# Kernel optimization log

Hardware: AMD Instinct MI355X
Metric: run time of the kernel (lower is better)

Reference implementation:

```python
import jax, jax.numpy as jnp
import numpy as np

B, T, E = 4, 2048, 1024
H, HS = 16, 64

def setup_inputs() -> dict:
    key = jax.random.key(0)
    ks = jax.random.split(key, 6)
    return {
        "x": jax.random.normal(ks[0], (B, T, E), dtype=jnp.float32),
        "Wq": jax.random.normal(ks[1], (H, E, HS), dtype=jnp.float32) * 0.02,
        "Wk": jax.random.normal(ks[2], (H, E, HS), dtype=jnp.float32) * 0.02,
        "Wv": jax.random.normal(ks[3], (H, E, HS), dtype=jnp.float32) * 0.02,
        "proj_w": jax.random.normal(ks[4], (E, H * HS), dtype=jnp.float32) * 0.02,
        "proj_b": jax.random.normal(ks[5], (E,), dtype=jnp.float32) * 0.02,
    }

def reference(x, Wq, Wk, Wv, proj_w, proj_b):
    b, t, e = x.shape
    h, _, hs = Wq.shape
    # NOTE: original uses .view() (raw reshape, not transpose) from [b,t,h,hs]
    # to [h,b,t,hs]; we replicate that exactly for faithfulness.
    q = jnp.einsum('bxy,iyk->bxik', x, Wq).reshape(h, b, t, hs)
    k = jnp.einsum('bxy,iyk->bxik', x, Wk).reshape(h, b, t, hs)
    v = jnp.einsum('bxy,iyk->bxik', x, Wv).reshape(h, b, t, hs)
    # scores: [h, b, t, t], scaled by 1/sqrt(head_size)
    wei = jnp.einsum('hbqd,hbkd->hbqk', q, k) * (hs ** -0.5)
    causal = jnp.tril(jnp.ones((t, t), dtype=bool))  # [t, t]
    wei = jnp.where(causal, wei, -jnp.inf)
    wei = jax.nn.softmax(wei, axis=-1)  # dropout is identity in eval
    out = jnp.einsum('hbqk,hbkd->hbqd', wei, v)
    # raw reshape [h,b,t,hs] -> [b,t,h*hs], matching torch .view()
    out = out.reshape(b, t, h * hs)
    out = out @ proj_w.T + proj_b  # nn.Linear
    return out
```

## Files before the change

### kernel.cpp

```cpp
#include <hip/hip_runtime.h>

typedef unsigned short u16;
typedef __attribute__((ext_vector_type(8))) __bf16 bf16x8;
typedef __attribute__((ext_vector_type(4))) float f32x4;
typedef __attribute__((ext_vector_type(16))) float f32x16;
typedef __attribute__((ext_vector_type(4))) unsigned short ushort4v;
typedef __attribute__((ext_vector_type(2))) unsigned uint2v;

__device__ __forceinline__ u16 f2bf(float f) {
  unsigned u = __builtin_bit_cast(unsigned, f);
  u += 0x7fffu + ((u >> 16) & 1u);
  return (u16)(u >> 16);
}

__device__ __forceinline__ float exp2_hw(float x) {
  float r; asm("v_exp_f32 %0, %1" : "=v"(r) : "v"(x)); return r;
}
__device__ __forceinline__ unsigned cvt_pk_bf16(float a, float b) {
  unsigned r; asm("v_cvt_pk_bf16_f32 %0, %1, %2" : "=v"(r) : "v"(a), "v"(b)); return r;
}

__device__ __forceinline__ void gload_lds16(const void* g, void* l) {
  __builtin_amdgcn_global_load_lds(
      (__attribute__((address_space(1))) void*)g,
      (__attribute__((address_space(3))) void*)l, 16, 0, 0);
}

__device__ __forceinline__ void BAR() {
  asm volatile("" ::: "memory");
  __builtin_amdgcn_s_barrier();
  asm volatile("" ::: "memory");
}

#define MFMA16(a, b, c) __builtin_amdgcn_mfma_f32_16x16x32_bf16(a, b, c, 0, 0, 0)
#define MFMA32(a, b, c) __builtin_amdgcn_mfma_f32_32x32x16_bf16(a, b, c, 0, 0, 0)

#define QSCALE 0.1803368801111204f


__global__ __launch_bounds__(256)
void prep_kernel(const float* __restrict__ x, const float* __restrict__ Wq,
                 const float* __restrict__ Wk, const float* __restrict__ Wv,
                 const float* __restrict__ pw, u16* __restrict__ Xb,
                 u16* __restrict__ Wcat, u16* __restrict__ PWt) {
  const int b = blockIdx.x, tid = threadIdx.x;
  if (b < 8192) {
    int i = b * 256 + tid;
    float4 v = ((const float4*)x)[i];
    union { u16 u[4]; uint2 v2; } r;
    r.u[0] = f2bf(v.x); r.u[1] = f2bf(v.y); r.u[2] = f2bf(v.z); r.u[3] = f2bf(v.w);
    ((uint2*)Xb)[i] = r.v2;
  } else if (b < 8960) {
    __shared__ u16 lds[64 * 68];
    int bb = b - 8192;
    int sel = bb >> 8, rem = bb & 255;
    int h = rem >> 4, e0 = (rem & 15) * 64;
    const float* W = (sel == 0) ? Wq : (sel == 1) ? Wk : Wv;
    const float* src = W + ((size_t)h * 1024 + e0) * 64;
#pragma unroll
    for (int i = 0; i < 4; i++) {
      int idx = i * 1024 + tid * 4;
      int e = idx >> 6, hs = idx & 63;
      float4 v = *(const float4*)&src[idx];
      u16* d = &lds[e * 68 + hs];
      d[0] = f2bf(v.x); d[1] = f2bf(v.y); d[2] = f2bf(v.z); d[3] = f2bf(v.w);
    }
    __syncthreads();
#pragma unroll
    for (int i = 0; i < 2; i++) {
      int u = i * 256 + tid;
      int hs = u >> 3, ec = u & 7;
      union { u16 q[8]; uint4 v; } ou;
#pragma unroll
      for (int e = 0; e < 8; e++) ou.q[e] = lds[(ec * 8 + e) * 68 + hs];
      size_t n = (size_t)sel * 1024 + h * 64 + hs;
      *(uint4*)&Wcat[n * 1024 + e0 + ec * 8] = ou.v;
    }
  } else {
    int i = (b - 8960) * 256 + tid;
    float4 v = ((const float4*)pw)[i];
    union { u16 u[4]; uint2 v2; } r;
    r.u[0] = f2bf(v.x); r.u[1] = f2bf(v.y); r.u[2] = f2bf(v.z); r.u[3] = f2bf(v.w);
    ((uint2*)PWt)[i] = r.v2;
  }
}


template<int OUT_BF16>
__global__ __launch_bounds__(512, 2)
void gemm3b(const u16* __restrict__ A, const u16* __restrict__ BT,
            void* __restrict__ Cout, const float* __restrict__ bias,
            int M, int N, int K, int qcols) {
  __shared__ u16 a_lds[3][128 * 64];
  __shared__ u16 b_lds[3][256 * 64];
  const int xcd = blockIdx.x & 7;
  const int local = blockIdx.x >> 3;
  const int by = xcd * 8 + (local & 7);
  const int bx = local >> 3;
  const int tid = threadIdx.x;
  const int lane = tid & 63;
  const int w = tid >> 6;
  const int wr = w >> 2, wc = w & 3;
  const int mBase = by * 128, nBase = bx * 256;
  const int l15 = lane & 15, l4 = lane >> 4;
  const int nkt = K >> 6;

  f32x4 acc[4][4] = {};

  auto STAGE_A = [&](int s, int kt) {
#pragma unroll
    for (int j = 0; j < 2; j++) {
      int e = j * 4096 + tid * 8;
      int row = e >> 6;
      int c = ((e >> 3) & 7) ^ (row & 7);
      gload_lds16(A + (size_t)(mBase + row) * K + kt * 64 + c * 8, &a_lds[s][e]);
    }
  };
  auto STAGE_B = [&](int s, int kt) {
#pragma unroll
    for (int j = 0; j < 4; j++) {
      int e = j * 4096 + tid * 8;
      int row = e >> 6;
      int c = ((e >> 3) & 7) ^ (row & 7);
      gload_lds16(BT + (size_t)(nBase + row) * K + kt * 64 + c * 8, &b_lds[s][e]);
    }
  };

  STAGE_A(0, 0); STAGE_B(0, 0);
  STAGE_A(1, 1); STAGE_B(1, 1);
  asm volatile("s_waitcnt vmcnt(6)" ::: "memory");
  BAR();

  int s0 = 0, s1 = 1, s2 = 2;
  for (int t = 0; t < nkt; t++) {
    const int t2 = (t + 2 < nkt) ? t + 2 : t + 2 - nkt;
    bf16x8 AF[4][2], BF[2][2];

#pragma unroll
    for (int m = 0; m < 4; m++) {
      int row = wr * 64 + m * 16 + l15;
#pragma unroll
      for (int ks = 0; ks < 2; ks++) {
        int ch = (ks * 4 + l4) ^ (row & 7);
        AF[m][ks] = *(const bf16x8*)&a_lds[s0][row * 64 + ch * 8];
      }
    }
#pragma unroll
    for (int n = 0; n < 2; n++) {
      int row = wc * 64 + n * 16 + l15;
#pragma unroll
      for (int ks = 0; ks < 2; ks++) {
        int ch = (ks * 4 + l4) ^ (row & 7);
        BF[n][ks] = *(const bf16x8*)&b_lds[s0][row * 64 + ch * 8];
      }
    }
    STAGE_A(s2, t2);
    BAR();
    __builtin_amdgcn_s_setprio(1);
#pragma unroll
    for (int m = 0; m < 4; m++)
#pragma unroll
      for (int n = 0; n < 2; n++) {
        acc[m][n] = MFMA16(AF[m][0], BF[n][0], acc[m][n]);
        acc[m][n] = MFMA16(AF[m][1], BF[n][1], acc[m][n]);
      }
    __builtin_amdgcn_s_setprio(0);

#pragma unroll
    for (int n = 0; n < 2; n++) {
      int row = wc * 64 + 32 + n * 16 + l15;
#pragma unroll
      for (int ks = 0; ks < 2; ks++) {
        int ch = (ks * 4 + l4) ^ (row & 7);
        BF[n][ks] = *(const bf16x8*)&b_lds[s0][row * 64 + ch * 8];
      }
    }
    STAGE_B(s2, t2);
    BAR();
    __builtin_amdgcn_s_setprio(1);
#pragma unroll
    for (int m = 0; m < 4; m++)
#pragma unroll
      for (int n = 0; n < 2; n++) {
        acc[m][2 + n] = MFMA16(AF[m][0], BF[n][0], acc[m][2 + n]);
        acc[m][2 + n] = MFMA16(AF[m][1], BF[n][1], acc[m][2 + n]);
      }
    __builtin_amdgcn_s_setprio(0);

    asm volatile("s_waitcnt vmcnt(6)" ::: "memory");
    BAR();
    int tmp = s0; s0 = s1; s1 = s2; s2 = tmp;
  }

#pragma unroll
  for (int mi = 0; mi < 4; mi++) {
    int row = mBase + wr * 64 + mi * 16 + l4 * 4;
#pragma unroll
    for (int ni = 0; ni < 4; ni++) {
      int col = nBase + wc * 64 + ni * 16 + l15;
      float scl = (col < qcols) ? QSCALE : 1.f;
#pragma unroll
      for (int j = 0; j < 4; j++) {
        float v = acc[mi][ni][j];
        if (OUT_BF16) {
          ((u16*)Cout)[(size_t)(row + j) * N + col] = f2bf(v * scl);
        } else {
          ((float*)Cout)[(size_t)(row + j) * N + col] = v + bias[col];
        }
      }
    }
  }
}


__global__ __launch_bounds__(256)
void vt_build(const u16* __restrict__ qkv, u16* __restrict__ vt) {
  __shared__ u16 lds[64 * 66];
  const int hb = blockIdx.x >> 5, tc = blockIdx.x & 31;
  const int t0 = tc * 64, tid = threadIdx.x;
#pragma unroll
  for (int i = 0; i < 2; i++) {
    int idx = i * 2048 + tid * 8;
    int tl = idx >> 6, d0 = idx & 63;
    int r = hb * 2048 + t0 + tl;
    const u16* src = &qkv[(size_t)(r >> 4) * 3072 + 2048 + (r & 15) * 64 + d0];
    uint4 v = *(const uint4*)src;
    u16* dst = &lds[tl * 66 + d0];
    *(unsigned*)(dst + 0) = v.x; *(unsigned*)(dst + 2) = v.y;
    *(unsigned*)(dst + 4) = v.z; *(unsigned*)(dst + 6) = v.w;
  }
  __syncthreads();
#pragma unroll
  for (int i = 0; i < 2; i++) {
    int idx = i * 2048 + tid * 8;
    int d = idx >> 6, tl0 = idx & 63;
    union { u16 u[8]; uint4 v; } ou;
#pragma unroll
    for (int e = 0; e < 8; e++) ou.u[e] = lds[(tl0 + e) * 66 + d];
    *(uint4*)&vt[(size_t)hb * 131072 + (size_t)d * 2048 + t0 + tl0] = ou.v;
  }
}


__global__ __launch_bounds__(256)
void attn_kernel(const u16* __restrict__ qkv, const u16* __restrict__ vtg,
                 u16* __restrict__ att) {
  __shared__ u16 k_lds[2][64 * 64];
  __shared__ u16 v_lds[2][64 * 64];

  const int xcd = blockIdx.x & 7;
  const int c = blockIdx.x >> 3;
  const int hb = xcd * 8 + (c & 7);
  const int qb = 15 - (c >> 3);
  const int tid = threadIdx.x;
  const int lane = tid & 63, w = tid >> 6;
  const int l31 = lane & 31, l5 = lane >> 5;
  const int qbase = qb * 128 + w * 32;
  const int nkt = 2 * qb + 2;

  bf16x8 qf[4];
  {
    int t = qbase + l31;
    int r = hb * 2048 + t;
    size_t base = (size_t)(r >> 4) * 3072 + (r & 15) * 64;
#pragma unroll
    for (int d = 0; d < 4; d++)
      qf[d] = *(const bf16x8*)&qkv[base + d * 16 + l5 * 8];
  }

  f32x16 o0 = {}, o1 = {};
  float lp = 0.f;

  auto STAGE = [&](int buf, int kt) {
#pragma unroll
    for (int i = 0; i < 2; i++) {
      int U = i * 2048 + tid * 8;
      int row = U >> 6;
      int chunk = ((U >> 3) & 7) ^ (row & 7);
      int rK = hb * 2048 + kt * 64 + row;
      gload_lds16(&qkv[(size_t)(rK >> 4) * 3072 + 1024 + (rK & 15) * 64 + chunk * 8],
                  &k_lds[buf][U]);
    }
#pragma unroll
    for (int i = 0; i < 2; i++) {
      int U = i * 2048 + tid * 8;
      int row = U >> 6;
      int chunk = ((U >> 3) & 7) ^ (row & 7);
      gload_lds16(&vtg[(size_t)hb * 131072 + (size_t)row * 2048 + kt * 64 + chunk * 8],
                  &v_lds[buf][U]);
    }
  };

  STAGE(0, 0);
  asm volatile("s_waitcnt vmcnt(0)" ::: "memory");
  BAR();

  for (int kt = 0; kt < nkt; kt++) {
    if (kt + 1 < nkt) STAGE((kt + 1) & 1, kt + 1);
    const int cur = kt & 1;
    const bool active = (kt * 64 <= qbase + 31);
    if (active) {
      const bool full = (kt * 64 + 63 <= qbase);
      const int q = qbase + l31;
#pragma unroll
      for (int kb = 0; kb < 2; kb++) {
        int krow = kb * 32 + l31;
        int ksw = krow & 7;
        f32x16 st = {};
        __builtin_amdgcn_s_setprio(1);
#pragma unroll
        for (int t = 0; t < 4; t++) {
          bf16x8 kf = *(const bf16x8*)&k_lds[cur][krow * 64 + ((t * 2 + l5) ^ ksw) * 8];
          st = MFMA32(kf, qf[t], st);
        }
        __builtin_amdgcn_s_setprio(0);
        float p[16];
#pragma unroll
        for (int r = 0; r < 16; r++) {
          float v = st[r];
          if (!full) {
            int k = kt * 64 + kb * 32 + (r & 3) + 8 * (r >> 2) + 4 * l5;
            v = (k > q) ? -INFINITY : v;
          }
          p[r] = exp2_hw(v);
        }
        float ps = (((p[0] + p[1]) + (p[2] + p[3])) + ((p[4] + p[5]) + (p[6] + p[7]))) +
                   (((p[8] + p[9]) + (p[10] + p[11])) + ((p[12] + p[13]) + (p[14] + p[15])));
        lp += ps;
#pragma unroll
        for (int kc = 0; kc < 2; kc++) {
          unsigned w0 = cvt_pk_bf16(p[kc * 8 + 0], p[kc * 8 + 1]);
          unsigned w1 = cvt_pk_bf16(p[kc * 8 + 2], p[kc * 8 + 3]);
          unsigned w2 = cvt_pk_bf16(p[kc * 8 + 4], p[kc * 8 + 5]);
          unsigned w3 = cvt_pk_bf16(p[kc * 8 + 6], p[kc * 8 + 7]);
          uint2v sw0 = __builtin_amdgcn_permlane32_swap(w0, w2, false, false);
          uint2v sw1 = __builtin_amdgcn_permlane32_swap(w1, w3, false, false);
          union { unsigned u[4]; bf16x8 v; } pf;
          pf.u[0] = sw0.x; pf.u[1] = sw1.x; pf.u[2] = sw0.y; pf.u[3] = sw1.y;
          __builtin_amdgcn_s_setprio(1);
          {
            int row0 = l31;
            int ch0 = (kb * 4 + kc * 2 + l5) ^ (row0 & 7);
            bf16x8 vf0 = *(const bf16x8*)&v_lds[cur][row0 * 64 + ch0 * 8];
            o0 = MFMA32(vf0, pf.v, o0);
            int row1 = 32 + l31;
            int ch1 = (kb * 4 + kc * 2 + l5) ^ (row1 & 7);
            bf16x8 vf1 = *(const bf16x8*)&v_lds[cur][row1 * 64 + ch1 * 8];
            o1 = MFMA32(vf1, pf.v, o1);
          }
          __builtin_amdgcn_s_setprio(0);
        }
      }
    }
    asm volatile("s_waitcnt vmcnt(0)" ::: "memory");
    BAR();
  }

  lp += __shfl_xor(lp, 32);
  float rl = 1.f / lp;
  {
    int q = qbase + l31;
    size_t rbase = ((size_t)hb * 2048 + q) * 64;
#pragma unroll
    for (int g = 0; g < 4; g++) {
      uint2 wv;
      wv.x = cvt_pk_bf16(o0[4 * g + 0] * rl, o0[4 * g + 1] * rl);
      wv.y = cvt_pk_bf16(o0[4 * g + 2] * rl, o0[4 * g + 3] * rl);
      *(uint2*)&att[rbase + g * 8 + 4 * l5] = wv;
      uint2 wu;
      wu.x = cvt_pk_bf16(o1[4 * g + 0] * rl, o1[4 * g + 1] * rl);
      wu.y = cvt_pk_bf16(o1[4 * g + 2] * rl, o1[4 * g + 3] * rl);
      *(uint2*)&att[rbase + 32 + g * 8 + 4 * l5] = wu;
    }
  }
}


extern "C" void kernel_launch(void* const* d_in, const int* in_sizes, int n_in,
                              void* d_out, int out_size, void* d_ws, size_t ws_size,
                              hipStream_t stream) {
  const float* x  = (const float*)d_in[0];
  const float* Wq = (const float*)d_in[1];
  const float* Wk = (const float*)d_in[2];
  const float* Wv = (const float*)d_in[3];
  const float* pw = (const float*)d_in[4];
  const float* pb = (const float*)d_in[5];
  float* out = (float*)d_out;

  char* ws = (char*)d_ws;
  u16* Xb   = (u16*)(ws);
  u16* VTg  = (u16*)(ws);
  u16* Wcat = (u16*)(ws + (16u << 20));
  u16* PWt  = (u16*)(ws + (22u << 20));
  u16* QKV  = (u16*)(ws + (24u << 20));
  u16* ATT  = (u16*)(ws + (72u << 20));

  prep_kernel<<<9984, 256, 0, stream>>>(x, Wq, Wk, Wv, pw, Xb, Wcat, PWt);

  gemm3b<1><<<768, 512, 0, stream>>>(Xb, Wcat, QKV, nullptr, 8192, 3072, 1024, 1024);

  vt_build<<<2048, 256, 0, stream>>>(QKV, VTg);

  attn_kernel<<<1024, 256, 0, stream>>>(QKV, VTg, ATT);

  gemm3b<0><<<256, 512, 0, stream>>>(ATT, PWt, out, pb, 8192, 1024, 1024, 0);
}
```

Baseline: 162.5 us.

## Split long causal query blocks across two workgroups and merge partial outputs

Query blocks 10-15, the longest causal rows, are split into two halves of the key range and run as separate workgroups. A lookup table orders the work items so long items are scheduled first. Each half writes an unnormalized bf16 partial output and its row sum, and a new merge kernel adds the two and normalizes. The aim is to balance the causal tail and raise parallelism, at the cost of an extra kernel launch, extra global traffic, and a second bf16 rounding of the partial outputs. Merging without per-row max correction relies on the kernel already using a fixed softmax offset instead of a running max.

```diff
diff --git a/kernel.cpp b/kernel.cpp
--- a/kernel.cpp
+++ b/kernel.cpp
@@ -4,7 +4,6 @@
 typedef __attribute__((ext_vector_type(8))) __bf16 bf16x8;
 typedef __attribute__((ext_vector_type(4))) float f32x4;
 typedef __attribute__((ext_vector_type(16))) float f32x16;
-typedef __attribute__((ext_vector_type(4))) unsigned short ushort4v;
 typedef __attribute__((ext_vector_type(2))) unsigned uint2v;
 
 __device__ __forceinline__ u16 f2bf(float f) {
@@ -12,20 +11,20 @@
   u += 0x7fffu + ((u >> 16) & 1u);
   return (u16)(u >> 16);
 }
-
+__device__ __forceinline__ float bf2f(u16 u) {
+  return __builtin_bit_cast(float, (unsigned)u << 16);
+}
 __device__ __forceinline__ float exp2_hw(float x) {
   float r; asm("v_exp_f32 %0, %1" : "=v"(r) : "v"(x)); return r;
 }
 __device__ __forceinline__ unsigned cvt_pk_bf16(float a, float b) {
   unsigned r; asm("v_cvt_pk_bf16_f32 %0, %1, %2" : "=v"(r) : "v"(a), "v"(b)); return r;
 }
-
 __device__ __forceinline__ void gload_lds16(const void* g, void* l) {
   __builtin_amdgcn_global_load_lds(
       (__attribute__((address_space(1))) void*)g,
       (__attribute__((address_space(3))) void*)l, 16, 0, 0);
 }
-
 __device__ __forceinline__ void BAR() {
   asm volatile("" ::: "memory");
   __builtin_amdgcn_s_barrier();
@@ -36,6 +35,9 @@
 #define MFMA32(a, b, c) __builtin_amdgcn_mfma_f32_32x32x16_bf16(a, b, c, 0, 0, 0)
 
 #define QSCALE 0.1803368801111204f
+
+__device__ const short ATAB_QB[22] = {9,8,15,15,7,14,14,6,13,13,5,12,12,4,11,11,3,10,10,2,1,0};
+__device__ const short ATAB_MD[22] = {0,0, 1, 2,0, 1, 2,0, 1, 2,0, 1, 2,0, 1, 2,0, 1, 2,0,0,0};
 
 
 __global__ __launch_bounds__(256)
@@ -244,19 +246,24 @@
 
 __global__ __launch_bounds__(256)
 void attn_kernel(const u16* __restrict__ qkv, const u16* __restrict__ vtg,
-                 u16* __restrict__ att) {
+                 u16* __restrict__ att, u16* __restrict__ o1b,
+                 float* __restrict__ L0, float* __restrict__ L1) {
   __shared__ u16 k_lds[2][64 * 64];
   __shared__ u16 v_lds[2][64 * 64];
 
   const int xcd = blockIdx.x & 7;
-  const int c = blockIdx.x >> 3;
-  const int hb = xcd * 8 + (c & 7);
-  const int qb = 15 - (c >> 3);
+  const int local = blockIdx.x >> 3;
+  const int hb = xcd * 8 + (local & 7);
+  const int item = local >> 3;
+  const int qb = ATAB_QB[item];
+  const int md = ATAB_MD[item];
   const int tid = threadIdx.x;
   const int lane = tid & 63, w = tid >> 6;
   const int l31 = lane & 31, l5 = lane >> 5;
   const int qbase = qb * 128 + w * 32;
   const int nkt = 2 * qb + 2;
+  const int KT0 = (md == 2) ? (nkt >> 1) : 0;
+  const int KT1 = (md == 1) ? (nkt >> 1) : nkt;
 
   bf16x8 qf[4];
   {
@@ -291,13 +298,14 @@
     }
   };
 
-  STAGE(0, 0);
+  STAGE(0, KT0);
   asm volatile("s_waitcnt vmcnt(0)" ::: "memory");
   BAR();
 
-  for (int kt = 0; kt < nkt; kt++) {
-    if (kt + 1 < nkt) STAGE((kt + 1) & 1, kt + 1);
-    const int cur = kt & 1;
+  for (int kt = KT0; kt < KT1; kt++) {
+    const int s = kt - KT0;
+    if (kt + 1 < KT1) STAGE((s + 1) & 1, kt + 1);
+    const int cur = s & 1;
     const bool active = (kt * 64 <= qbase + 31);
     if (active) {
       const bool full = (kt * 64 + 63 <= qbase);
@@ -357,10 +365,9 @@
   }
 
   lp += __shfl_xor(lp, 32);
-  float rl = 1.f / lp;
-  {
-    int q = qbase + l31;
-    size_t rbase = ((size_t)hb * 2048 + q) * 64;
+  if (md == 0) {
+    float rl = 1.f / lp;
+    size_t rbase = ((size_t)hb * 2048 + qbase + l31) * 64;
 #pragma unroll
     for (int g = 0; g < 4; g++) {
       uint2 wv;
@@ -372,7 +379,52 @@
       wu.y = cvt_pk_bf16(o1[4 * g + 2] * rl, o1[4 * g + 3] * rl);
       *(uint2*)&att[rbase + 32 + g * 8 + 4 * l5] = wu;
     }
-  }
+  } else {
+    const int slotrow = ((qb - 10) * 64 + hb) * 128 + w * 32 + l31;
+    u16* dst;
+    size_t rbase;
+    if (md == 1) {
+      rbase = ((size_t)hb * 2048 + qbase + l31) * 64;
+      dst = att;
+      if (l5 == 0) L0[slotrow] = lp;
+    } else {
+      rbase = (size_t)slotrow * 64;
+      dst = o1b;
+      if (l5 == 0) L1[slotrow] = lp;
+    }
+#pragma unroll
+    for (int g = 0; g < 4; g++) {
+      uint2 wv;
+      wv.x = cvt_pk_bf16(o0[4 * g + 0], o0[4 * g + 1]);
+      wv.y = cvt_pk_bf16(o0[4 * g + 2], o0[4 * g + 3]);
+      *(uint2*)&dst[rbase + g * 8 + 4 * l5] = wv;
+      uint2 wu;
+      wu.x = cvt_pk_bf16(o1[4 * g + 0], o1[4 * g + 1]);
+      wu.y = cvt_pk_bf16(o1[4 * g + 2], o1[4 * g + 3]);
+      *(uint2*)&dst[rbase + 32 + g * 8 + 4 * l5] = wu;
+    }
+  }
+}
+
+
+__global__ __launch_bounds__(256)
+void attn_merge(u16* __restrict__ att, const u16* __restrict__ o1b,
+                const float* __restrict__ L0, const float* __restrict__ L1) {
+  int gid = blockIdx.x * 256 + threadIdx.x;
+  int row = gid >> 3;
+  int dc = (gid & 7) * 8;
+  int sqb = row >> 13;
+  int rem = row & 8191;
+  int hb = rem >> 7;
+  int qrow = rem & 127;
+  size_t arow = ((size_t)hb * 2048 + (10 + sqb) * 128 + qrow) * 64 + dc;
+  float rl = 1.f / (L0[row] + L1[row]);
+  union { u16 u[8]; uint4 v; } a, b, o;
+  a.v = *(const uint4*)&att[arow];
+  b.v = *(const uint4*)&o1b[(size_t)row * 64 + dc];
+#pragma unroll
+  for (int i = 0; i < 8; i++) o.u[i] = f2bf((bf2f(a.u[i]) + bf2f(b.u[i])) * rl);
+  *(uint4*)&att[arow] = o.v;
 }
 
 
@@ -391,9 +443,12 @@
   u16* Xb   = (u16*)(ws);
   u16* VTg  = (u16*)(ws);
   u16* Wcat = (u16*)(ws + (16u << 20));
+  u16* O1b  = (u16*)(ws + (16u << 20));
   u16* PWt  = (u16*)(ws + (22u << 20));
   u16* QKV  = (u16*)(ws + (24u << 20));
   u16* ATT  = (u16*)(ws + (72u << 20));
+  float* L0 = (float*)(ws + (88u << 20));
+  float* L1 = (float*)(ws + (88u << 20) + (192u << 10));
 
   prep_kernel<<<9984, 256, 0, stream>>>(x, Wq, Wk, Wv, pw, Xb, Wcat, PWt);
 
@@ -401,7 +456,9 @@
 
   vt_build<<<2048, 256, 0, stream>>>(QKV, VTg);
 
-  attn_kernel<<<1024, 256, 0, stream>>>(QKV, VTg, ATT);
+  attn_kernel<<<1408, 256, 0, stream>>>(QKV, VTg, ATT, O1b, L0, L1);
+
+  attn_merge<<<1536, 256, 0, stream>>>(ATT, O1b, L0, L1);
 
   gemm3b<0><<<256, 512, 0, stream>>>(ATT, PWt, out, pb, 8192, 1024, 1024, 0);
 }
```

After: 167.0 us. +2.8%, slower.

## Reshape GEMM block tile to 256x128 with four-phase MFMA/load interleave

Applied to the files above, without the earlier changes.

The shared GEMM kernel moves from a 128x256 block tile to 256x128, and its eight waves are rearranged from a 2x4 grid to a 4x2 grid. Each k-step is split into four MFMA quadrants, with A-half, A-half and B loads issued between them and barriers separating each phase. The XCD-aware block mapping and the staging helpers are adjusted to the new tile shape, and a final vmcnt(0) drains the wrap-around prefetches. The goal is a better balance of LDS fragment reads against MFMA work and finer-grained overlap of global-to-LDS loads, at the cost of extra barriers per iteration.

```diff
diff --git a/kernel.cpp b/kernel.cpp
--- a/kernel.cpp
+++ b/kernel.cpp
@@ -4,7 +4,6 @@
 typedef __attribute__((ext_vector_type(8))) __bf16 bf16x8;
 typedef __attribute__((ext_vector_type(4))) float f32x4;
 typedef __attribute__((ext_vector_type(16))) float f32x16;
-typedef __attribute__((ext_vector_type(4))) unsigned short ushort4v;
 typedef __attribute__((ext_vector_type(2))) unsigned uint2v;
 
 __device__ __forceinline__ u16 f2bf(float f) {
@@ -12,20 +11,17 @@
   u += 0x7fffu + ((u >> 16) & 1u);
   return (u16)(u >> 16);
 }
-
 __device__ __forceinline__ float exp2_hw(float x) {
   float r; asm("v_exp_f32 %0, %1" : "=v"(r) : "v"(x)); return r;
 }
 __device__ __forceinline__ unsigned cvt_pk_bf16(float a, float b) {
   unsigned r; asm("v_cvt_pk_bf16_f32 %0, %1, %2" : "=v"(r) : "v"(a), "v"(b)); return r;
 }
-
 __device__ __forceinline__ void gload_lds16(const void* g, void* l) {
   __builtin_amdgcn_global_load_lds(
       (__attribute__((address_space(1))) void*)g,
       (__attribute__((address_space(3))) void*)l, 16, 0, 0);
 }
-
 __device__ __forceinline__ void BAR() {
   asm volatile("" ::: "memory");
   __builtin_amdgcn_s_barrier();
@@ -88,116 +84,150 @@
 
 template<int OUT_BF16>
 __global__ __launch_bounds__(512, 2)
-void gemm3b(const u16* __restrict__ A, const u16* __restrict__ BT,
+void gemm4p(const u16* __restrict__ A, const u16* __restrict__ BT,
             void* __restrict__ Cout, const float* __restrict__ bias,
             int M, int N, int K, int qcols) {
-  __shared__ u16 a_lds[3][128 * 64];
-  __shared__ u16 b_lds[3][256 * 64];
+  __shared__ u16 a_lds[3][256 * 64];
+  __shared__ u16 b_lds[3][128 * 64];
   const int xcd = blockIdx.x & 7;
   const int local = blockIdx.x >> 3;
-  const int by = xcd * 8 + (local & 7);
-  const int bx = local >> 3;
+  const int by = xcd * 4 + (local & 3);
+  const int bx = local >> 2;
   const int tid = threadIdx.x;
   const int lane = tid & 63;
   const int w = tid >> 6;
-  const int wr = w >> 2, wc = w & 3;
-  const int mBase = by * 128, nBase = bx * 256;
+  const int wm = w >> 1, wn = w & 1;
+  const int mBase = by * 256, nBase = bx * 128;
   const int l15 = lane & 15, l4 = lane >> 4;
   const int nkt = K >> 6;
 
   f32x4 acc[4][4] = {};
 
-  auto STAGE_A = [&](int s, int kt) {
+  auto STAGE_A2 = [&](int s, int kt, int j0) {
+#pragma unroll
+    for (int j = 0; j < 2; j++) {
+      int e = (j0 + j) * 4096 + tid * 8;
+      int row = e >> 6;
+      int c = ((e >> 3) & 7) ^ (row & 7);
+      gload_lds16(A + (size_t)(mBase + row) * K + kt * 64 + c * 8, &a_lds[s][e]);
+    }
+  };
+  auto STAGE_B2 = [&](int s, int kt) {
 #pragma unroll
     for (int j = 0; j < 2; j++) {
       int e = j * 4096 + tid * 8;
       int row = e >> 6;
       int c = ((e >> 3) & 7) ^ (row & 7);
-      gload_lds16(A + (size_t)(mBase + row) * K + kt * 64 + c * 8, &a_lds[s][e]);
+      gload_lds16(BT + (size_t)(nBase + row) * K + kt * 64 + c * 8, &b_lds[s][e]);
     }
   };
-  auto STAGE_B = [&](int s, int kt) {
-#pragma unroll
-    for (int j = 0; j < 4; j++) {
-      int e = j * 4096 + tid * 8;
-      int row = e >> 6;
-      int c = ((e >> 3) & 7) ^ (row & 7);
-      gload_lds16(BT + (size_t)(nBase + row) * K + kt * 64 + c * 8, &b_lds[s][e]);
-    }
-  };
-
-  STAGE_A(0, 0); STAGE_B(0, 0);
-  STAGE_A(1, 1); STAGE_B(1, 1);
+
+  STAGE_A2(0, 0, 0); STAGE_A2(0, 0, 2); STAGE_B2(0, 0);
+  STAGE_A2(1, 1, 0); STAGE_A2(1, 1, 2); STAGE_B2(1, 1);
   asm volatile("s_waitcnt vmcnt(6)" ::: "memory");
   BAR();
 
   int s0 = 0, s1 = 1, s2 = 2;
   for (int t = 0; t < nkt; t++) {
     const int t2 = (t + 2 < nkt) ? t + 2 : t + 2 - nkt;
-    bf16x8 AF[4][2], BF[2][2];
-
-#pragma unroll
-    for (int m = 0; m < 4; m++) {
-      int row = wr * 64 + m * 16 + l15;
+    bf16x8 AF0[2][2], AF1[2][2], BF0[2][2], BF1[2][2];
+
+#pragma unroll
+    for (int mm = 0; mm < 2; mm++) {
+      int row = wm * 64 + mm * 16 + l15;
 #pragma unroll
       for (int ks = 0; ks < 2; ks++) {
         int ch = (ks * 4 + l4) ^ (row & 7);
-        AF[m][ks] = *(const bf16x8*)&a_lds[s0][row * 64 + ch * 8];
-      }
-    }
-#pragma unroll
-    for (int n = 0; n < 2; n++) {
-      int row = wc * 64 + n * 16 + l15;
+        AF0[mm][ks] = *(const bf16x8*)&a_lds[s0][row * 64 + ch * 8];
+      }
+    }
+#pragma unroll
+    for (int nn = 0; nn < 2; nn++) {
+      int row = wn * 64 + nn * 16 + l15;
 #pragma unroll
       for (int ks = 0; ks < 2; ks++) {
         int ch = (ks * 4 + l4) ^ (row & 7);
-        BF[n][ks] = *(const bf16x8*)&b_lds[s0][row * 64 + ch * 8];
-      }
-    }
-    STAGE_A(s2, t2);
+        BF0[nn][ks] = *(const bf16x8*)&b_lds[s0][row * 64 + ch * 8];
+      }
+    }
+    STAGE_A2(s2, t2, 0);
     BAR();
     __builtin_amdgcn_s_setprio(1);
 #pragma unroll
-    for (int m = 0; m < 4; m++)
-#pragma unroll
-      for (int n = 0; n < 2; n++) {
-        acc[m][n] = MFMA16(AF[m][0], BF[n][0], acc[m][n]);
-        acc[m][n] = MFMA16(AF[m][1], BF[n][1], acc[m][n]);
+    for (int mm = 0; mm < 2; mm++)
+#pragma unroll
+      for (int nn = 0; nn < 2; nn++) {
+        acc[mm][nn] = MFMA16(AF0[mm][0], BF0[nn][0], acc[mm][nn]);
+        acc[mm][nn] = MFMA16(AF0[mm][1], BF0[nn][1], acc[mm][nn]);
       }
     __builtin_amdgcn_s_setprio(0);
-
-#pragma unroll
-    for (int n = 0; n < 2; n++) {
-      int row = wc * 64 + 32 + n * 16 + l15;
+    BAR();
+
+#pragma unroll
+    for (int nn = 0; nn < 2; nn++) {
+      int row = wn * 64 + 32 + nn * 16 + l15;
 #pragma unroll
       for (int ks = 0; ks < 2; ks++) {
         int ch = (ks * 4 + l4) ^ (row & 7);
-        BF[n][ks] = *(const bf16x8*)&b_lds[s0][row * 64 + ch * 8];
-      }
-    }
-    STAGE_B(s2, t2);
+        BF1[nn][ks] = *(const bf16x8*)&b_lds[s0][row * 64 + ch * 8];
+      }
+    }
+    STAGE_A2(s2, t2, 2);
     BAR();
     __builtin_amdgcn_s_setprio(1);
 #pragma unroll
-    for (int m = 0; m < 4; m++)
-#pragma unroll
-      for (int n = 0; n < 2; n++) {
-        acc[m][2 + n] = MFMA16(AF[m][0], BF[n][0], acc[m][2 + n]);
-        acc[m][2 + n] = MFMA16(AF[m][1], BF[n][1], acc[m][2 + n]);
+    for (int mm = 0; mm < 2; mm++)
+#pragma unroll
+      for (int nn = 0; nn < 2; nn++) {
+        acc[mm][2 + nn] = MFMA16(AF0[mm][0], BF1[nn][0], acc[mm][2 + nn]);
+        acc[mm][2 + nn] = MFMA16(AF0[mm][1], BF1[nn][1], acc[mm][2 + nn]);
       }
     __builtin_amdgcn_s_setprio(0);
-
+    BAR();
+
+#pragma unroll
+    for (int mm = 0; mm < 2; mm++) {
+      int row = wm * 64 + 32 + mm * 16 + l15;
+#pragma unroll
+      for (int ks = 0; ks < 2; ks++) {
+        int ch = (ks * 4 + l4) ^ (row & 7);
+        AF1[mm][ks] = *(const bf16x8*)&a_lds[s0][row * 64 + ch * 8];
+      }
+    }
+    STAGE_B2(s2, t2);
+    BAR();
+    __builtin_amdgcn_s_setprio(1);
+#pragma unroll
+    for (int mm = 0; mm < 2; mm++)
+#pragma unroll
+      for (int nn = 0; nn < 2; nn++) {
+        acc[2 + mm][nn] = MFMA16(AF1[mm][0], BF0[nn][0], acc[2 + mm][nn]);
+        acc[2 + mm][nn] = MFMA16(AF1[mm][1], BF0[nn][1], acc[2 + mm][nn]);
+      }
+    __builtin_amdgcn_s_setprio(0);
+    BAR();
+
+    __builtin_amdgcn_s_setprio(1);
+#pragma unroll
+    for (int mm = 0; mm < 2; mm++)
+#pragma unroll
+      for (int nn = 0; nn < 2; nn++) {
+        acc[2 + mm][2 + nn] = MFMA16(AF1[mm][0], BF1[nn][0], acc[2 + mm][2 + nn]);
+        acc[2 + mm][2 + nn] = MFMA16(AF1[mm][1], BF1[nn][1], acc[2 + mm][2 + nn]);
+      }
+    __builtin_amdgcn_s_setprio(0);
     asm volatile("s_waitcnt vmcnt(6)" ::: "memory");
     BAR();
     int tmp = s0; s0 = s1; s1 = s2; s2 = tmp;
   }
+  asm volatile("s_waitcnt vmcnt(0)" ::: "memory");
 
 #pragma unroll
   for (int mi = 0; mi < 4; mi++) {
-    int row = mBase + wr * 64 + mi * 16 + l4 * 4;
+    int row = mBase + wm * 64 + mi * 16 + l4 * 4;
 #pragma unroll
     for (int ni = 0; ni < 4; ni++) {
-      int col = nBase + wc * 64 + ni * 16 + l15;
+      int col = nBase + wn * 64 + ni * 16 + l15;
       float scl = (col < qcols) ? QSCALE : 1.f;
 #pragma unroll
       for (int j = 0; j < 4; j++) {
@@ -397,11 +427,11 @@
 
   prep_kernel<<<9984, 256, 0, stream>>>(x, Wq, Wk, Wv, pw, Xb, Wcat, PWt);
 
-  gemm3b<1><<<768, 512, 0, stream>>>(Xb, Wcat, QKV, nullptr, 8192, 3072, 1024, 1024);
+  gemm4p<1><<<768, 512, 0, stream>>>(Xb, Wcat, QKV, nullptr, 8192, 3072, 1024, 1024);
 
   vt_build<<<2048, 256, 0, stream>>>(QKV, VTg);
 
   attn_kernel<<<1024, 256, 0, stream>>>(QKV, VTg, ATT);
 
-  gemm3b<0><<<256, 512, 0, stream>>>(ATT, PWt, out, pb, 8192, 1024, 1024, 0);
-}
+  gemm4p<0><<<256, 512, 0, stream>>>(ATT, PWt, out, pb, 8192, 1024, 1024, 0);
+}
```

New measurement: 176.5 us. 8.6% more time.
